# Performance work log

Hardware: AMD Instinct MI355X
Metric: run time of the kernel (lower is better)

## Reference

```python
import jax, jax.numpy as jnp
import numpy as np

EMB = 512
HEADS = 16
WH, WW = 8, 8
N = WH * WW
B = 2048
CPB_HID = 512
EPS = 1e-12


def _buffers():
    # continuous relative coords table, shape (1, 2*WH-1, 2*WW-1, 2)
    ch = np.arange(-(WH - 1), WH, dtype=np.float32)
    cw = np.arange(-(WW - 1), WW, dtype=np.float32)
    t = np.stack(np.meshgrid(ch, cw, indexing='ij')).transpose(1, 2, 0)[None].copy()
    t[..., 0] /= (WH - 1)
    t[..., 1] /= (WW - 1)
    t *= 8.0
    t = np.sign(t) * np.log2(np.abs(t) + 1.0) / np.log2(8.0)
    # relative position index, shape (N, N), values in [0, (2*WH-1)*(2*WW-1))
    coords = np.stack(np.meshgrid(np.arange(WH), np.arange(WW), indexing='ij'))
    cf = coords.reshape(2, -1)
    rel = (cf[:, :, None] - cf[:, None, :]).transpose(1, 2, 0).copy()
    rel[..., 0] += WH - 1
    rel[..., 1] += WW - 1
    rel[..., 0] *= 2 * WW - 1
    idx = rel.sum(-1)
    return jnp.asarray(t, jnp.float32), jnp.asarray(idx, jnp.int32)


def setup_inputs() -> dict:
    key = jax.random.key(0)
    ks = jax.random.split(key, 8)
    rel_table, rel_index = _buffers()
    s = 0.02
    return {
        'x': jax.random.normal(ks[0], (B, N, EMB), jnp.float32),
        'qkv_w': jax.random.normal(ks[1], (3 * EMB, EMB), jnp.float32) * s,
        'q_bias': jnp.zeros((EMB,), jnp.float32),
        'v_bias': jnp.zeros((EMB,), jnp.float32),
        'flex_attn': jnp.full((HEADS, 1, 1), np.log(10.0), jnp.float32),
        'cpb_w1': jax.random.normal(ks[2], (CPB_HID, 2), jnp.float32) * s,
        'cpb_b1': jnp.zeros((CPB_HID,), jnp.float32),
        'cpb_w2': jax.random.normal(ks[3], (HEADS, CPB_HID), jnp.float32) * s,
        'proj_w': jax.random.normal(ks[4], (EMB, EMB), jnp.float32) * s,
        'proj_b': jnp.zeros((EMB,), jnp.float32),
        'rel_table': rel_table,
        'rel_index': rel_index,
    }


def reference(x, qkv_w, q_bias, v_bias, flex_attn, cpb_w1, cpb_b1, cpb_w2,
              proj_w, proj_b, rel_table, rel_index):
    Bx, Nx, C = x.shape
    H = HEADS
    D = C // H
    # qkv with bias only on q and v (k bias is zero), as in the torch code
    qkv_bias = jnp.concatenate([q_bias, jnp.zeros_like(v_bias), v_bias])
    qkv = x @ qkv_w.T + qkv_bias                      # (B, N, 3C)
    qkv = qkv.reshape(Bx, Nx, 3, H, D).transpose(2, 0, 3, 1, 4)
    q, k, v = qkv[0], qkv[1], qkv[2]                  # each (B, H, N, D)
    # cosine attention: L2-normalize q and k
    qn = q / jnp.maximum(jnp.linalg.norm(q, axis=-1, keepdims=True), EPS)
    kn = k / jnp.maximum(jnp.linalg.norm(k, axis=-1, keepdims=True), EPS)
    attn = jnp.einsum('bhnd,bhmd->bhnm', qn, kn)      # (B, H, N, N)
    # learned per-head temperature, clamped at 1/0.01
    scale = jnp.exp(jnp.minimum(flex_attn, jnp.log(jnp.float32(100.0))))  # (H,1,1)
    attn = attn * scale[None]
    # continuous relative position bias via MLP + gather
    bias_tab = jax.nn.relu(rel_table @ cpb_w1.T + cpb_b1) @ cpb_w2.T      # (1, 2WH-1, 2WW-1, H)
    bias_tab = bias_tab.reshape(-1, H)
    bias = bias_tab[rel_index.reshape(-1)].reshape(Nx, Nx, H)
    bias = 16.0 * jax.nn.sigmoid(bias.transpose(2, 0, 1))                 # (H, N, N)
    attn = jax.nn.softmax(attn + bias[None], axis=-1)
    out = jnp.einsum('bhnm,bhmd->bhnd', attn, v)      # (B, H, N, D)
    out = out.transpose(0, 2, 1, 3).reshape(Bx, Nx, C)
    return out @ proj_w.T + proj_b
```

## Files before the change

kernel.cpp:

```cpp
#include <hip/hip_runtime.h>

using bf16x8 = __attribute__((ext_vector_type(8))) short;
using f32x4  = __attribute__((ext_vector_type(4))) float;

static constexpr int EMB = 512, HEADS = 16, NTOK = 64, BWIN = 2048;
static constexpr int MROWS = BWIN * NTOK;
static constexpr int QKVN  = 3 * EMB;

__device__ __forceinline__ float bf2f(unsigned int u) {
  union { unsigned int i; float f; } c; c.i = u << 16; return c.f;
}
__device__ __forceinline__ unsigned short f2bf(float x) {
  union { float f; unsigned int i; } c; c.f = x;
  return (unsigned short)((c.i + 0x7fffu + ((c.i >> 16) & 1u)) >> 16);
}
__device__ __forceinline__ void gload_lds16(const void* g, void* l) {
  __builtin_amdgcn_global_load_lds((const __attribute__((address_space(1))) void*)g,
                                   (__attribute__((address_space(3))) void*)l, 16, 0, 0);
}

#define BARRIER() __builtin_amdgcn_s_barrier()
#define LGKM0()  do { asm volatile("s_waitcnt lgkmcnt(0)" ::: "memory"); \
                      __builtin_amdgcn_sched_barrier(0); } while (0)
#define VMCNT2() do { asm volatile("s_waitcnt vmcnt(2)" ::: "memory"); \
                      __builtin_amdgcn_sched_barrier(0); } while (0)

__global__ __launch_bounds__(256) void xcast(const float* __restrict__ x,
                                             unsigned short* __restrict__ xb) {
  size_t i = ((size_t)blockIdx.x * 256 + threadIdx.x) * 8;
  float4 a = *(const float4*)(x + i);
  float4 b = *(const float4*)(x + i + 4);
  ushort4 lo = make_ushort4(f2bf(a.x), f2bf(a.y), f2bf(a.z), f2bf(a.w));
  ushort4 hi = make_ushort4(f2bf(b.x), f2bf(b.y), f2bf(b.z), f2bf(b.w));
  *(ushort4*)(xb + i) = lo;
  *(ushort4*)(xb + i + 4) = hi;
}

__global__ void prep_weights(const float* __restrict__ qkv_w, const float* __restrict__ proj_w,
                             const float* __restrict__ q_bias, const float* __restrict__ v_bias,
                             unsigned short* __restrict__ wq, unsigned short* __restrict__ wp,
                             float* __restrict__ qkv_bias) {
  int i = blockIdx.x * 256 + threadIdx.x;
  wq[i] = f2bf(qkv_w[i]);
  if (i < EMB * EMB) wp[i] = f2bf(proj_w[i]);
  if (i < EMB) {
    qkv_bias[i]           = q_bias[i];
    qkv_bias[EMB + i]     = 0.f;
    qkv_bias[2 * EMB + i] = v_bias[i];
  }
}

__global__ __launch_bounds__(64) void cpb_mlp(const float* __restrict__ tbl,
                        const float* __restrict__ w1, const float* __restrict__ b1,
                        const float* __restrict__ w2, float* __restrict__ tab) {
  __shared__ float hid[512];
  const int p = blockIdx.x, t = threadIdx.x;
  const float t0 = tbl[p * 2], t1 = tbl[p * 2 + 1];
  #pragma unroll
  for (int s = 0; s < 8; ++s) {
    int j = t + s * 64;
    hid[j] = fmaxf(0.f, t0 * w1[j * 2] + t1 * w1[j * 2 + 1] + b1[j]);
  }
  __syncthreads();
  const int h = t >> 2, q = t & 3;
  float sum = 0.f;
  for (int j = q * 128; j < q * 128 + 128; ++j) sum += hid[j] * w2[h * 512 + j];
  sum += __shfl_xor(sum, 1);
  sum += __shfl_xor(sum, 2);
  if (q == 0) tab[p * 16 + h] = sum;
}

__global__ void cpb_expand(const float* __restrict__ tab, const int* __restrict__ rel_index,
                           float* __restrict__ bias16) {
  int e = blockIdx.x * 256 + threadIdx.x;
  int h = e >> 12, ij = e & 4095;
  float x = tab[rel_index[ij] * 16 + h];
  bias16[e] = 16.f / (1.f + __expf(-x));
}

template<bool OUT_F32, int NBX, int KT>
__global__ __launch_bounds__(512, 2) void gemm256(const unsigned short* __restrict__ Ap,
    const unsigned short* __restrict__ Bp, const float* __restrict__ bias,
    void* __restrict__ Cp, int M, int N) {
  __shared__ unsigned short As[2][256 * 64];
  __shared__ unsigned short Bs[2][256 * 64];
  constexpr int NT = KT / 64;
  constexpr int NITER = NT / 2;
  const int t = threadIdx.x;
  const int l = t & 63, w = t >> 6;
  const int lr = l & 15, lg = l >> 4;
  const int q8 = gridDim.x >> 3;
  const int wgid = (blockIdx.x & 7) * q8 + (blockIdx.x >> 3);
  const int n0 = (wgid % NBX) * 256, m0 = (wgid / NBX) * 256;
  const int wm = (w >> 2) * 128, wn = (w & 3) * 64;
  const int ha128 = (w >> 2) * 128;
  const int srow = t >> 3;
  const int scol = ((t & 7) ^ (srow & 7)) << 3;
  const unsigned short* Abase = Ap + (size_t)m0 * KT;
  const unsigned short* Bbase = Bp + (size_t)n0 * KT;

  f32x4 acc[8][4];
  #pragma unroll
  for (int i = 0; i < 8; ++i)
    #pragma unroll
    for (int j = 0; j < 4; ++j) acc[i][j] = (f32x4){0.f, 0.f, 0.f, 0.f};
  bf16x8 afr[4][2], bfr[4][2];

  auto stage_half = [&](int d, int kt, int half, bool isA) {
    const unsigned short* g = (isA ? Abase : Bbase)
        + (size_t)(half * 128 + srow) * KT + kt * 64 + scol;
    unsigned short* lds = (isA ? &As[d][0] : &Bs[d][0]) + half * 8192 + (t >> 6) * 512;
    gload_lds16(g, lds);
    gload_lds16(g + (size_t)64 * KT, lds + 4096);
  };
  auto ldA4 = [&](int d, int mb) {
    #pragma unroll
    for (int m = 0; m < 4; ++m) {
      int row = ha128 + (mb + m) * 16 + lr;
      #pragma unroll
      for (int ks = 0; ks < 2; ++ks)
        afr[m][ks] = *(const bf16x8*)(&As[d][row * 64 + ((((ks << 2) + lg) ^ (lr & 7)) << 3)]);
    }
  };
  auto ldB2 = [&](int d, int nb) {
    #pragma unroll
    for (int n = 0; n < 2; ++n) {
      int row = wn + (nb + n) * 16 + lr;
      #pragma unroll
      for (int ks = 0; ks < 2; ++ks)
        bfr[nb + n][ks] = *(const bf16x8*)(&Bs[d][row * 64 + ((((ks << 2) + lg) ^ (lr & 7)) << 3)]);
    }
  };
  auto mfmaQ = [&](int mb, int nb) {
    __builtin_amdgcn_s_setprio(1);
    #pragma unroll
    for (int ks = 0; ks < 2; ++ks)
      #pragma unroll
      for (int m = 0; m < 4; ++m)
        #pragma unroll
        for (int n = 0; n < 2; ++n)
          acc[mb + m][nb + n] = __builtin_amdgcn_mfma_f32_16x16x32_bf16(
              afr[m][ks], bfr[nb + n][ks], acc[mb + m][nb + n], 0, 0, 0);
    __builtin_amdgcn_s_setprio(0);
  };

  stage_half(0, 0, 0, true);  stage_half(0, 0, 1, true);
  stage_half(0, 0, 0, false); stage_half(0, 0, 1, false);
  stage_half(1, (NT > 1 ? 1 : 0), 0, true);
  VMCNT2();
  BARRIER();

  for (int i = 0; i < NITER; ++i) {
    const int kt1 = 2 * i + 1;
    const int kt2 = (2 * i + 2 < NT) ? 2 * i + 2 : NT - 1;
    const int kt3 = (2 * i + 3 < NT) ? 2 * i + 3 : NT - 1;
    ldA4(0, 0); ldB2(0, 0);
    stage_half(1, kt1, 1, true);
    BARRIER(); LGKM0(); mfmaQ(0, 0); BARRIER();
    ldB2(0, 2);
    stage_half(1, kt1, 0, false);
    BARRIER(); LGKM0(); mfmaQ(0, 2); BARRIER();
    ldA4(0, 4);
    stage_half(1, kt1, 1, false);
    BARRIER(); LGKM0(); mfmaQ(4, 2); BARRIER();
    stage_half(0, kt2, 0, true);
    VMCNT2(); BARRIER(); mfmaQ(4, 0); BARRIER();
    ldA4(1, 0); ldB2(1, 0);
    stage_half(0, kt2, 1, true);
    BARRIER(); LGKM0(); mfmaQ(0, 0); BARRIER();
    ldB2(1, 2);
    stage_half(0, kt2, 0, false);
    BARRIER(); LGKM0(); mfmaQ(0, 2); BARRIER();
    ldA4(1, 4);
    stage_half(0, kt2, 1, false);
    BARRIER(); LGKM0(); mfmaQ(4, 2); BARRIER();
    stage_half(1, kt3, 0, true);
    VMCNT2(); BARRIER(); mfmaQ(4, 0); BARRIER();
  }

  #pragma unroll
  for (int mf = 0; mf < 8; ++mf)
    #pragma unroll
    for (int nf = 0; nf < 4; ++nf)
      #pragma unroll
      for (int r = 0; r < 4; ++r) {
        int mm = m0 + wm + mf * 16 + lg * 4 + r;
        int nn = n0 + wn + nf * 16 + lr;
        float v = acc[mf][nf][r] + bias[nn];
        if (OUT_F32) ((float*)Cp)[(size_t)mm * N + nn] = v;
        else ((unsigned short*)Cp)[(size_t)mm * N + nn] = f2bf(v);
      }
}

__device__ __forceinline__ bf16x8 load_norm_frag(const unsigned short* p, float s) {
  uint4 raw = *(const uint4*)p;
  float f[8];
  f[0] = bf2f(raw.x & 0xffffu); f[1] = bf2f(raw.x >> 16);
  f[2] = bf2f(raw.y & 0xffffu); f[3] = bf2f(raw.y >> 16);
  f[4] = bf2f(raw.z & 0xffffu); f[5] = bf2f(raw.z >> 16);
  f[6] = bf2f(raw.w & 0xffffu); f[7] = bf2f(raw.w >> 16);
  float ss = 0.f;
  #pragma unroll
  for (int j = 0; j < 8; ++j) ss += f[j] * f[j];
  ss += __shfl_xor(ss, 16);
  ss += __shfl_xor(ss, 32);
  float inv = s / fmaxf(sqrtf(ss), 1e-12f);
  bf16x8 v;
  #pragma unroll
  for (int j = 0; j < 8; ++j) v[j] = (short)f2bf(f[j] * inv);
  return v;
}

__global__ __launch_bounds__(128) void attn_win(const unsigned short* __restrict__ qkv,
    const float* __restrict__ bias16, const float* __restrict__ flex,
    unsigned short* __restrict__ aout) {
  __shared__ float sS[2][64 * 65];
  __shared__ unsigned short sP[2][64 * 72];
  __shared__ float sRs[2][64];
  const int w = threadIdx.x >> 6, l = threadIdx.x & 63;
  const int lr = l & 15, lg = l >> 4;
  const int b = blockIdx.x >> 3;
  const int h = ((blockIdx.x & 7) << 1) | w;
  const unsigned short* base = qkv + (size_t)b * NTOK * QKVN;
  const float scale = __expf(fminf(flex[h], 4.6051701860f));

  bf16x8 aq[4], bk[4];
  #pragma unroll
  for (int i = 0; i < 4; ++i)
    aq[i] = load_norm_frag(base + (size_t)(i * 16 + lr) * QKVN + h * 32 + lg * 8, scale);
  #pragma unroll
  for (int i = 0; i < 4; ++i)
    bk[i] = load_norm_frag(base + (size_t)(i * 16 + lr) * QKVN + EMB + h * 32 + lg * 8, 1.f);

  const f32x4 z = (f32x4){0.f, 0.f, 0.f, 0.f};
  f32x4 sacc[4][4];
  #pragma unroll
  for (int i = 0; i < 4; ++i)
    #pragma unroll
    for (int j = 0; j < 4; ++j)
      sacc[i][j] = __builtin_amdgcn_mfma_f32_16x16x32_bf16(aq[i], bk[j], z, 0, 0, 0);

  float* S = sS[w];
  const float* bh = bias16 + (size_t)h * 4096;
  #pragma unroll
  for (int i = 0; i < 4; ++i)
    #pragma unroll
    for (int j = 0; j < 4; ++j)
      #pragma unroll
      for (int r = 0; r < 4; ++r) {
        int row = i * 16 + lg * 4 + r, col = j * 16 + lr;
        S[row * 65 + col] = sacc[i][j][r] + bh[row * 64 + col];
      }
  __syncthreads();

  float rowv[64];
  float mx = -1e30f;
  #pragma unroll
  for (int j = 0; j < 64; ++j) { rowv[j] = S[l * 65 + j]; mx = fmaxf(mx, rowv[j]); }
  float sum = 0.f;
  unsigned short* P = sP[w];
  #pragma unroll
  for (int j = 0; j < 64; ++j) {
    float e = __expf(rowv[j] - mx);
    sum += e;
    P[l * 72 + j] = f2bf(e);
  }
  sRs[w][l] = 1.f / sum;
  __syncthreads();

  unsigned short* vT = (unsigned short*)sS[w];
  {
    const uint4* vp = (const uint4*)(base + (size_t)l * QKVN + 2 * EMB + h * 32);
    uint4 r0 = vp[0], r1 = vp[1], r2 = vp[2], r3 = vp[3];
    unsigned int wd[16] = {r0.x, r0.y, r0.z, r0.w, r1.x, r1.y, r1.z, r1.w,
                           r2.x, r2.y, r2.z, r2.w, r3.x, r3.y, r3.z, r3.w};
    #pragma unroll
    for (int d = 0; d < 32; ++d) {
      unsigned short val = (d & 1) ? (unsigned short)(wd[d >> 1] >> 16)
                                   : (unsigned short)(wd[d >> 1] & 0xffffu);
      vT[d * 72 + l] = val;
    }
  }
  __syncthreads();

  f32x4 oacc[4][2];
  #pragma unroll
  for (int i = 0; i < 4; ++i) { oacc[i][0] = z; oacc[i][1] = z; }
  #pragma unroll
  for (int ks = 0; ks < 2; ++ks) {
    bf16x8 ap[4], bv[2];
    #pragma unroll
    for (int i = 0; i < 4; ++i)
      ap[i] = *(const bf16x8*)(P + (i * 16 + lr) * 72 + ks * 32 + lg * 8);
    #pragma unroll
    for (int jd = 0; jd < 2; ++jd)
      bv[jd] = *(const bf16x8*)(vT + (jd * 16 + lr) * 72 + ks * 32 + lg * 8);
    #pragma unroll
    for (int i = 0; i < 4; ++i)
      #pragma unroll
      for (int jd = 0; jd < 2; ++jd)
        oacc[i][jd] = __builtin_amdgcn_mfma_f32_16x16x32_bf16(ap[i], bv[jd], oacc[i][jd], 0, 0, 0);
  }
  #pragma unroll
  for (int i = 0; i < 4; ++i)
    #pragma unroll
    for (int jd = 0; jd < 2; ++jd)
      #pragma unroll
      for (int r = 0; r < 4; ++r) {
        int tok = i * 16 + lg * 4 + r, d = jd * 16 + lr;
        float val = oacc[i][jd][r] * sRs[w][tok];
        aout[(size_t)(b * NTOK + tok) * EMB + h * 32 + d] = f2bf(val);
      }
}

extern "C" void kernel_launch(void* const* d_in, const int* in_sizes, int n_in,
                              void* d_out, int out_size, void* d_ws, size_t ws_size,
                              hipStream_t stream) {
  const float* x         = (const float*)d_in[0];
  const float* qkv_w     = (const float*)d_in[1];
  const float* q_bias    = (const float*)d_in[2];
  const float* v_bias    = (const float*)d_in[3];
  const float* flex      = (const float*)d_in[4];
  const float* cpb_w1    = (const float*)d_in[5];
  const float* cpb_b1    = (const float*)d_in[6];
  const float* cpb_w2    = (const float*)d_in[7];
  const float* proj_w    = (const float*)d_in[8];
  const float* proj_b    = (const float*)d_in[9];
  const float* rel_table = (const float*)d_in[10];
  const int*   rel_index = (const int*)d_in[11];

  char* ws = (char*)d_ws;
  unsigned short* qkv_bf = (unsigned short*)(ws + 0);
  unsigned short* xb     = (unsigned short*)(ws + 402653184ull);
  unsigned short* ao_bf  = (unsigned short*)(ws + 402653184ull);
  unsigned short* wq_bf  = (unsigned short*)(ws + 536870912ull);
  unsigned short* wp_bf  = (unsigned short*)(ws + 538443776ull);
  float* qkv_bias        = (float*)(ws + 538968064ull);
  float* tab             = (float*)(ws + 538974208ull);
  float* bias16          = (float*)(ws + 538988608ull);

  xcast<<<32768, 256, 0, stream>>>(x, xb);
  prep_weights<<<3072, 256, 0, stream>>>(qkv_w, proj_w, q_bias, v_bias, wq_bf, wp_bf, qkv_bias);
  cpb_mlp<<<225, 64, 0, stream>>>(rel_table, cpb_w1, cpb_b1, cpb_w2, tab);
  cpb_expand<<<256, 256, 0, stream>>>(tab, rel_index, bias16);
  gemm256<false, 6, EMB><<<3072, 512, 0, stream>>>(
      xb, wq_bf, qkv_bias, (void*)qkv_bf, MROWS, QKVN);
  attn_win<<<BWIN * 8, 128, 0, stream>>>(qkv_bf, bias16, flex, ao_bf);
  gemm256<true, 2, EMB><<<1024, 512, 0, stream>>>(
      ao_bf, wp_bf, proj_b, d_out, MROWS, EMB);
}
```

Measured before the change: 680.0 us.

## Run windowed attention as one wave per block without barriers

Each (window, head) pair now gets its own 64-thread block instead of packing two heads into a 128-thread block. Because a block is a single wave, the __syncthreads calls become compiler memory fences, and the score, probability and transposed-V buffers share one smaller LDS region. The V loads are issued at kernel start so their latency overlaps the QK work. Probabilities are stored as 16-byte vectors, the softmax reciprocal is broadcast with a shuffle rather than through LDS, and the block index is remapped so consecutive blocks touch different windows. The design relies on LDS operations staying in order within a wave, and the smaller blocks add per-block scheduling overhead.

```diff
diff --git a/kernel.cpp b/kernel.cpp
--- a/kernel.cpp
+++ b/kernel.cpp
@@ -211,19 +211,24 @@
   return v;
 }
 
-__global__ __launch_bounds__(128) void attn_win(const unsigned short* __restrict__ qkv,
+__global__ __launch_bounds__(64, 2) void attn_win(const unsigned short* __restrict__ qkv,
     const float* __restrict__ bias16, const float* __restrict__ flex,
     unsigned short* __restrict__ aout) {
-  __shared__ float sS[2][64 * 65];
-  __shared__ unsigned short sP[2][64 * 72];
-  __shared__ float sRs[2][64];
-  const int w = threadIdx.x >> 6, l = threadIdx.x & 63;
+  __shared__ __align__(16) char smem[16640];
+  float* S           = (float*)smem;
+  unsigned short* P  = (unsigned short*)smem;
+  unsigned short* vT = (unsigned short*)(smem + 9216);
+  const int l = threadIdx.x;
   const int lr = l & 15, lg = l >> 4;
-  const int b = blockIdx.x >> 3;
-  const int h = ((blockIdx.x & 7) << 1) | w;
+  const int g = (blockIdx.x & 7) * (gridDim.x >> 3) + (blockIdx.x >> 3);
+  const int b = g >> 4;
+  const int h = g & 15;
   const unsigned short* base = qkv + (size_t)b * NTOK * QKVN;
   const float scale = __expf(fminf(flex[h], 4.6051701860f));
 
+  const uint4* vp = (const uint4*)(base + (size_t)l * QKVN + 2 * EMB + h * 32);
+  uint4 v0 = vp[0], v1 = vp[1], v2 = vp[2], v3 = vp[3];
+
   bf16x8 aq[4], bk[4];
   #pragma unroll
   for (int i = 0; i < 4; ++i)
@@ -240,7 +245,6 @@
     for (int j = 0; j < 4; ++j)
       sacc[i][j] = __builtin_amdgcn_mfma_f32_16x16x32_bf16(aq[i], bk[j], z, 0, 0, 0);
 
-  float* S = sS[w];
   const float* bh = bias16 + (size_t)h * 4096;
   #pragma unroll
   for (int i = 0; i < 4; ++i)
@@ -251,29 +255,29 @@
         int row = i * 16 + lg * 4 + r, col = j * 16 + lr;
         S[row * 65 + col] = sacc[i][j][r] + bh[row * 64 + col];
       }
-  __syncthreads();
 
   float rowv[64];
   float mx = -1e30f;
   #pragma unroll
   for (int j = 0; j < 64; ++j) { rowv[j] = S[l * 65 + j]; mx = fmaxf(mx, rowv[j]); }
+  asm volatile("" ::: "memory");
   float sum = 0.f;
-  unsigned short* P = sP[w];
-  #pragma unroll
-  for (int j = 0; j < 64; ++j) {
-    float e = __expf(rowv[j] - mx);
-    sum += e;
-    P[l * 72 + j] = f2bf(e);
-  }
-  sRs[w][l] = 1.f / sum;
-  __syncthreads();
-
-  unsigned short* vT = (unsigned short*)sS[w];
+  #pragma unroll
+  for (int s = 0; s < 8; ++s) {
+    bf16x8 pk;
+    #pragma unroll
+    for (int m = 0; m < 8; ++m) {
+      float e = __expf(rowv[s * 8 + m] - mx);
+      sum += e;
+      pk[m] = (short)f2bf(e);
+    }
+    *(bf16x8*)(P + l * 72 + s * 8) = pk;
+  }
+  const float inv = 1.f / sum;
+
   {
-    const uint4* vp = (const uint4*)(base + (size_t)l * QKVN + 2 * EMB + h * 32);
-    uint4 r0 = vp[0], r1 = vp[1], r2 = vp[2], r3 = vp[3];
-    unsigned int wd[16] = {r0.x, r0.y, r0.z, r0.w, r1.x, r1.y, r1.z, r1.w,
-                           r2.x, r2.y, r2.z, r2.w, r3.x, r3.y, r3.z, r3.w};
+    unsigned int wd[16] = {v0.x, v0.y, v0.z, v0.w, v1.x, v1.y, v1.z, v1.w,
+                           v2.x, v2.y, v2.z, v2.w, v3.x, v3.y, v3.z, v3.w};
     #pragma unroll
     for (int d = 0; d < 32; ++d) {
       unsigned short val = (d & 1) ? (unsigned short)(wd[d >> 1] >> 16)
@@ -281,7 +285,7 @@
       vT[d * 72 + l] = val;
     }
   }
-  __syncthreads();
+  asm volatile("" ::: "memory");
 
   f32x4 oacc[4][2];
   #pragma unroll
@@ -308,7 +312,7 @@
       #pragma unroll
       for (int r = 0; r < 4; ++r) {
         int tok = i * 16 + lg * 4 + r, d = jd * 16 + lr;
-        float val = oacc[i][jd][r] * sRs[w][tok];
+        float val = oacc[i][jd][r] * __shfl(inv, tok);
         aout[(size_t)(b * NTOK + tok) * EMB + h * 32 + d] = f2bf(val);
       }
 }
@@ -345,7 +349,7 @@
   cpb_expand<<<256, 256, 0, stream>>>(tab, rel_index, bias16);
   gemm256<false, 6, EMB><<<3072, 512, 0, stream>>>(
       xb, wq_bf, qkv_bias, (void*)qkv_bf, MROWS, QKVN);
-  attn_win<<<BWIN * 8, 128, 0, stream>>>(qkv_bf, bias16, flex, ao_bf);
+  attn_win<<<BWIN * HEADS, 64, 0, stream>>>(qkv_bf, bias16, flex, ao_bf);
   gemm256<true, 2, EMB><<<1024, 512, 0, stream>>>(
       ao_bf, wp_bf, proj_b, d_out, MROWS, EMB);
 }
```

New measurement: 644.7 us. 5.2% less time.
